# Performance work log

Measured on AMD Instinct MI355X. Metric: run time of the kernel, lower is better.

The kernel has to match this reference:

```python
import jax, jax.numpy as jnp
import numpy as np

N, E = 50000, 800000
IN_DIM, OUT_DIM, REL_DIM = 128, 64, 32
NEG_SLOPE = 0.01  # torch F.leaky_relu default


def setup_inputs() -> dict:
    key = jax.random.key(0)
    ks = jax.random.split(key, 12)
    return {
        "h": jax.random.normal(ks[0], (N, IN_DIM), jnp.float32),
        "relation": jax.random.normal(ks[1], (E, REL_DIM), jnp.float32),
        "score": jax.random.normal(ks[2], (E, 1), jnp.float32),
        "timestamp": jax.random.normal(ks[3], (E, 1), jnp.float32),
        "src": jax.random.randint(ks[4], (E,), 0, N, jnp.int32),
        "dst": jax.random.randint(ks[5], (E,), 0, N, jnp.int32),
        "W_n": jax.random.normal(ks[6], (IN_DIM, OUT_DIM), jnp.float32) / np.sqrt(IN_DIM),
        "W_r": jax.random.normal(ks[7], (REL_DIM, OUT_DIM), jnp.float32) / np.sqrt(REL_DIM),
        "W_s": jax.random.normal(ks[8], (1, OUT_DIM), jnp.float32),
        "W_t": jax.random.normal(ks[9], (1, OUT_DIM), jnp.float32),
        "a": jax.random.normal(ks[10], (5 * OUT_DIM,), jnp.float32) / np.sqrt(5 * OUT_DIM),
    }


def reference(h, relation, score, timestamp, src, dst, W_n, W_r, W_s, W_t, a):
    D = W_n.shape[1]
    z = h @ W_n                     # (N, D)
    er = relation @ W_r             # (E, D)
    es = score @ W_s                # (E, D)
    et = timestamp @ W_t            # (E, D)
    z_src = z[src]                  # (E, D) gather
    z_dst = z[dst]                  # (E, D) gather
    # attn_fc on concat([z_src, z_dst, er, es, et]) == sum of slice dot-products
    a1, a2, a3, a4, a5 = (a[0:D], a[D:2*D], a[2*D:3*D], a[3*D:4*D], a[4*D:5*D])
    logit = z_src @ a1 + z_dst @ a2 + er @ a3 + es @ a4 + et @ a5  # (E,)
    logit = jnp.where(logit >= 0, logit, NEG_SLOPE * logit)        # leaky_relu
    # segment softmax over edges grouped by dst node
    n = z.shape[0]
    seg_max = jax.ops.segment_max(logit, dst, num_segments=n)     # (N,)
    ex = jnp.exp(logit - seg_max[dst])                             # (E,)
    seg_sum = jax.ops.segment_sum(ex, dst, num_segments=n)        # (N,)
    alpha = ex / seg_sum[dst]                                      # (E,)
    # weighted scatter-sum of source features to dst nodes
    h_out = jax.ops.segment_sum(alpha[:, None] * z_src, dst, num_segments=n)  # (N, D)
    return h_out
```

## Files before the change

### kernel.cpp

```cpp
#include <hip/hip_runtime.h>

#define IN_DIM 128
#define OUT_DIM 64
#define REL_DIM 32
#define NEG_SLOPE 0.01f
#define CAP 64
#define FB_EDGES 2048
#define BCAP 1536
#define MAXB 1024

__global__ __launch_bounds__(256) void k_node(const float* __restrict__ h,
                                              const float* __restrict__ W_n,
                                              const float* __restrict__ a,
                                              float* __restrict__ z,
                                              float* __restrict__ s1,
                                              float* __restrict__ s2,
                                              int* __restrict__ bcnt, int n) {
    __shared__ float hs[IN_DIM * 65];
    __shared__ float s1p[4][64], s2p[4][64];
    int base = blockIdx.x * 64;

    if (blockIdx.x == 0)
        for (int i = threadIdx.x; i < MAXB; i += 256) bcnt[i] = 0;

    for (int i = threadIdx.x; i < 64 * 32; i += 256) {
        int r = i >> 5;
        int c4 = i & 31;
        float4 v = make_float4(0.f, 0.f, 0.f, 0.f);
        if (base + r < n) v = ((const float4*)(h + (size_t)(base + r) * IN_DIM))[c4];
        int k0 = c4 * 4;
        hs[(k0 + 0) * 65 + r] = v.x;
        hs[(k0 + 1) * 65 + r] = v.y;
        hs[(k0 + 2) * 65 + r] = v.z;
        hs[(k0 + 3) * 65 + r] = v.w;
    }
    __syncthreads();

    int lane = threadIdx.x & 63;
    int w = __builtin_amdgcn_readfirstlane(threadIdx.x >> 6);
    int c0 = w * 16;
    int row = base + lane;

    float acc[16];
    #pragma unroll
    for (int j = 0; j < 16; ++j) acc[j] = 0.f;

    const float* __restrict__ Wslice = W_n + c0;
    #pragma unroll 4
    for (int k = 0; k < IN_DIM; ++k) {
        float hv = hs[k * 65 + lane];
        const float* __restrict__ Wr = Wslice + k * OUT_DIM;
        #pragma unroll
        for (int j = 0; j < 16; ++j) acc[j] = fmaf(hv, Wr[j], acc[j]);
    }

    float p1 = 0.f, p2 = 0.f;
    #pragma unroll
    for (int j = 0; j < 16; ++j) {
        p1 = fmaf(acc[j], a[c0 + j], p1);
        p2 = fmaf(acc[j], a[OUT_DIM + c0 + j], p2);
    }
    s1p[w][lane] = p1;
    s2p[w][lane] = p2;

    if (row < n) {
        float4* zp = (float4*)(z + (size_t)row * OUT_DIM + c0);
        zp[0] = make_float4(acc[0], acc[1], acc[2], acc[3]);
        zp[1] = make_float4(acc[4], acc[5], acc[6], acc[7]);
        zp[2] = make_float4(acc[8], acc[9], acc[10], acc[11]);
        zp[3] = make_float4(acc[12], acc[13], acc[14], acc[15]);
    }
    __syncthreads();
    if (threadIdx.x < 64 && base + (int)threadIdx.x < n) {
        int l = threadIdx.x;
        s1[base + l] = s1p[0][l] + s1p[1][l] + s1p[2][l] + s1p[3][l];
        s2[base + l] = s2p[0][l] + s2p[1][l] + s2p[2][l] + s2p[3][l];
    }
}

__global__ __launch_bounds__(512) void k_fillP(const float* __restrict__ rel,
                                               const float* __restrict__ score,
                                               const float* __restrict__ ts,
                                               const int* __restrict__ src,
                                               const int* __restrict__ dst,
                                               const float* __restrict__ s1,
                                               const float* __restrict__ s2,
                                               const float* __restrict__ W_r,
                                               const float* __restrict__ W_s,
                                               const float* __restrict__ W_t,
                                               const float* __restrict__ a,
                                               int* __restrict__ bcnt,
                                               int2* __restrict__ rec2,
                                               int E, int nbkt) {
    __shared__ float cw[REL_DIM + 2];
    __shared__ int2  stage[FB_EDGES];
    __shared__ int   sinfo[FB_EDGES];
    __shared__ int   lhist[MAXB];
    __shared__ int   lbase[MAXB];
    int tid = threadIdx.x;

    if (tid < REL_DIM) {
        const float* a3 = a + 2 * OUT_DIM;
        float acc = 0.f;
        #pragma unroll
        for (int d2 = 0; d2 < OUT_DIM; ++d2)
            acc = fmaf(W_r[tid * OUT_DIM + d2], a3[d2], acc);
        cw[tid] = acc;
    } else if (tid == 32) {
        float acc = 0.f;
        for (int d2 = 0; d2 < OUT_DIM; ++d2) acc = fmaf(W_s[d2], a[3 * OUT_DIM + d2], acc);
        cw[32] = acc;
    } else if (tid == 33) {
        float acc = 0.f;
        for (int d2 = 0; d2 < OUT_DIM; ++d2) acc = fmaf(W_t[d2], a[4 * OUT_DIM + d2], acc);
        cw[33] = acc;
    }
    for (int i = tid; i < nbkt; i += 512) lhist[i] = 0;
    __syncthreads();

    int e0 = blockIdx.x * FB_EDGES;
    int g = tid >> 3;
    int sub = tid & 7;

    #pragma unroll 1
    for (int it = 0; it < FB_EDGES / 64; ++it) {
        int le = it * 64 + g;
        int e = e0 + le;
        if (e < E) {
            float4 w4 = ((const float4*)cw)[sub];
            float4 v = ((const float4*)rel)[(size_t)e * 8 + sub];
            float dot = v.x * w4.x + v.y * w4.y + v.z * w4.z + v.w * w4.w;
            dot += __shfl_xor(dot, 1, 8);
            dot += __shfl_xor(dot, 2, 8);
            dot += __shfl_xor(dot, 4, 8);
            if (sub == 0) {
                int s = src[e], d = dst[e];
                float lg = dot + s1[s] + s2[d] + score[e] * cw[32] + ts[e] * cw[33];
                lg = (lg >= 0.f) ? lg : NEG_SLOPE * lg;
                int b = d >> 6;
                int lr = atomicAdd(&lhist[b], 1);
                stage[le] = make_int2((int)(((unsigned)d << 16) | (unsigned)s),
                                      __float_as_int(lg));
                sinfo[le] = (lr << 12) | b;
            }
        }
    }
    __syncthreads();

    for (int b = tid; b < nbkt; b += 512) {
        int c = lhist[b];
        if (c > 0) lbase[b] = atomicAdd(bcnt + b, c);
    }
    __syncthreads();

    for (int le = tid; le < FB_EDGES; le += 512) {
        int e = e0 + le;
        if (e < E) {
            int info = sinfo[le];
            int b = info & 0xFFF;
            int lr = info >> 12;
            int pos = lbase[b] + lr;
            if (pos < BCAP) rec2[(size_t)b * BCAP + pos] = stage[le];
        }
    }
}

__global__ __launch_bounds__(256) void k_out2(const int* __restrict__ bcnt,
                                              const int2* __restrict__ rec2,
                                              const float* __restrict__ z,
                                              float* __restrict__ out, int n) {
    __shared__ int2 seg[64][CAP];
    __shared__ int scnt[64];
    int b = blockIdx.x;
    int tid = threadIdx.x;
    if (tid < 64) scnt[tid] = 0;
    __syncthreads();

    int cnt = bcnt[b];
    if (cnt > BCAP) cnt = BCAP;
    const int2* rb = rec2 + (size_t)b * BCAP;
    for (int i = tid; i < cnt; i += 256) {
        int2 r = rb[i];
        int dl = (int)((((unsigned)r.x) >> 16) & 63u);
        int rk = atomicAdd(&scnt[dl], 1);
        if (rk < CAP) seg[dl][rk] = make_int2(r.x & 0xffff, r.y);
    }
    __syncthreads();

    int lane = tid & 63;
    int w = tid >> 6;
    int eg = lane >> 4;
    int dl4 = lane & 15;
    for (int k = 0; k < 16; ++k) {
        int dl = w * 16 + k;
        int node = b * 64 + dl;
        if (node >= n) break;
        int deg = min(scnt[dl], CAP);
        float4 acc = make_float4(0.f, 0.f, 0.f, 0.f);
        if (deg > 0) {
            int2 pe = make_int2(0, (int)0xff800000u);
            if (lane < deg) pe = seg[dl][lane];
            float v = __int_as_float(pe.y);
            float m = v;
            #pragma unroll
            for (int o = 32; o > 0; o >>= 1) m = fmaxf(m, __shfl_xor(m, o, 64));
            float ex = __expf(v - m);
            float ssum = ex;
            #pragma unroll
            for (int o = 32; o > 0; o >>= 1) ssum += __shfl_xor(ssum, o, 64);
            float alpha = ex * (1.0f / ssum);
            for (int j0 = 0; j0 < deg; j0 += 4) {
                int j = j0 + eg;
                int jc = (j < 64) ? j : 63;
                float wj = __shfl(alpha, jc, 64);
                int sj = __shfl(pe.x, jc, 64);
                if (j < deg) {
                    float4 zv = ((const float4*)(z + (size_t)sj * OUT_DIM))[dl4];
                    acc.x = fmaf(wj, zv.x, acc.x);
                    acc.y = fmaf(wj, zv.y, acc.y);
                    acc.z = fmaf(wj, zv.z, acc.z);
                    acc.w = fmaf(wj, zv.w, acc.w);
                }
            }
        }
        #pragma unroll
        for (int o = 16; o <= 32; o <<= 1) {
            acc.x += __shfl_xor(acc.x, o, 64);
            acc.y += __shfl_xor(acc.y, o, 64);
            acc.z += __shfl_xor(acc.z, o, 64);
            acc.w += __shfl_xor(acc.w, o, 64);
        }
        if (eg == 0) ((float4*)(out + (size_t)node * OUT_DIM))[dl4] = acc;
    }
}

extern "C" void kernel_launch(void* const* d_in, const int* in_sizes, int n_in,
                              void* d_out, int out_size, void* d_ws, size_t ws_size,
                              hipStream_t stream) {
    const float* h         = (const float*)d_in[0];
    const float* relation  = (const float*)d_in[1];
    const float* score     = (const float*)d_in[2];
    const float* timestamp = (const float*)d_in[3];
    const int*   src       = (const int*)d_in[4];
    const int*   dst       = (const int*)d_in[5];
    const float* W_n       = (const float*)d_in[6];
    const float* W_r       = (const float*)d_in[7];
    const float* W_s       = (const float*)d_in[8];
    const float* W_t       = (const float*)d_in[9];
    const float* a         = (const float*)d_in[10];

    int n = in_sizes[0] / IN_DIM;
    int E = in_sizes[4];
    int nbkt = (n + 63) >> 6;

    float* ws   = (float*)d_ws;
    float* z    = ws;
    float* s1   = z + (size_t)n * OUT_DIM;
    float* s2   = s1 + n;
    int*   bcnt = (int*)(s2 + n);
    int2*  rec2 = (int2*)(bcnt + MAXB);

    float* out = (float*)d_out;

    k_node<<<(n + 63) / 64, 256, 0, stream>>>(h, W_n, a, z, s1, s2, bcnt, n);

    int nfb = (E + FB_EDGES - 1) / FB_EDGES;
    k_fillP<<<nfb, 512, 0, stream>>>(relation, score, timestamp, src, dst,
                                     s1, s2, W_r, W_s, W_t, a, bcnt, rec2, E, nbkt);

    k_out2<<<nbkt, 256, 0, stream>>>(bcnt, rec2, z, out, n);
}
```

Baseline: 297.8 us.

## Replace atomic bucket fill with histogram, scan and deterministic scatter passes

Edge bucketing by destination block now runs in three stages: a per-block histogram kernel, a per-bucket exclusive scan across edge blocks, and a scatter kernel that writes records straight to their precomputed offsets. This removes the global atomics on bucket counters and the second shared-memory staging pass. The scatter kernel also preloads src, dst, score and timestamp into shared memory. The output kernel moves to 512 threads with 8 nodes per wave. The cost is two extra launches and a scan kernel that does 1024-thread block syncs for each of about 782 buckets. The fixed HSTRIDE of 800 caps the node count.

```diff
diff --git a/kernel.cpp b/kernel.cpp
--- a/kernel.cpp
+++ b/kernel.cpp
@@ -5,23 +5,19 @@
 #define REL_DIM 32
 #define NEG_SLOPE 0.01f
 #define CAP 64
-#define FB_EDGES 2048
+#define EPB 1024
 #define BCAP 1536
-#define MAXB 1024
+#define HSTRIDE 800
 
 __global__ __launch_bounds__(256) void k_node(const float* __restrict__ h,
                                               const float* __restrict__ W_n,
                                               const float* __restrict__ a,
                                               float* __restrict__ z,
                                               float* __restrict__ s1,
-                                              float* __restrict__ s2,
-                                              int* __restrict__ bcnt, int n) {
+                                              float* __restrict__ s2, int n) {
     __shared__ float hs[IN_DIM * 65];
     __shared__ float s1p[4][64], s2p[4][64];
     int base = blockIdx.x * 64;
-
-    if (blockIdx.x == 0)
-        for (int i = threadIdx.x; i < MAXB; i += 256) bcnt[i] = 0;
 
     for (int i = threadIdx.x; i < 64 * 32; i += 256) {
         int r = i >> 5;
@@ -78,53 +74,101 @@
     }
 }
 
-__global__ __launch_bounds__(512) void k_fillP(const float* __restrict__ rel,
-                                               const float* __restrict__ score,
-                                               const float* __restrict__ ts,
-                                               const int* __restrict__ src,
-                                               const int* __restrict__ dst,
-                                               const float* __restrict__ s1,
-                                               const float* __restrict__ s2,
-                                               const float* __restrict__ W_r,
-                                               const float* __restrict__ W_s,
-                                               const float* __restrict__ W_t,
-                                               const float* __restrict__ a,
-                                               int* __restrict__ bcnt,
-                                               int2* __restrict__ rec2,
-                                               int E, int nbkt) {
-    __shared__ float cw[REL_DIM + 2];
-    __shared__ int2  stage[FB_EDGES];
-    __shared__ int   sinfo[FB_EDGES];
-    __shared__ int   lhist[MAXB];
-    __shared__ int   lbase[MAXB];
-    int tid = threadIdx.x;
-
-    if (tid < REL_DIM) {
+__global__ __launch_bounds__(256) void k_hist(const int* __restrict__ dst,
+                                              int* __restrict__ hist, int E, int nbkt) {
+    __shared__ int lh[HSTRIDE];
+    int t = threadIdx.x;
+    for (int i = t; i < nbkt; i += 256) lh[i] = 0;
+    __syncthreads();
+    int e0 = blockIdx.x * EPB;
+    #pragma unroll
+    for (int i = 0; i < EPB / 256; ++i) {
+        int e = e0 + i * 256 + t;
+        if (e < E) atomicAdd(&lh[dst[e] >> 6], 1);
+    }
+    __syncthreads();
+    for (int b = t; b < nbkt; b += 256)
+        hist[(size_t)blockIdx.x * HSTRIDE + b] = lh[b];
+}
+
+__global__ __launch_bounds__(1024) void k_scan(int* __restrict__ hist,
+                                               int* __restrict__ bcnt, int nblk) {
+    __shared__ int tmp[1024];
+    int b = blockIdx.x;
+    int t = threadIdx.x;
+    int v = (t < nblk) ? hist[(size_t)t * HSTRIDE + b] : 0;
+    tmp[t] = v;
+    __syncthreads();
+    #pragma unroll
+    for (int o = 1; o < 1024; o <<= 1) {
+        int x = (t >= o) ? tmp[t - o] : 0;
+        __syncthreads();
+        tmp[t] += x;
+        __syncthreads();
+    }
+    if (t < nblk) hist[(size_t)t * HSTRIDE + b] = tmp[t] - v;
+    if (t == 0) bcnt[b] = tmp[1023];
+}
+
+__global__ __launch_bounds__(256) void k_scatter(const float* __restrict__ rel,
+                                                 const float* __restrict__ score,
+                                                 const float* __restrict__ ts,
+                                                 const int* __restrict__ src,
+                                                 const int* __restrict__ dst,
+                                                 const float* __restrict__ s1,
+                                                 const float* __restrict__ s2,
+                                                 const float* __restrict__ W_r,
+                                                 const float* __restrict__ W_s,
+                                                 const float* __restrict__ W_t,
+                                                 const float* __restrict__ a,
+                                                 const int* __restrict__ hist,
+                                                 int2* __restrict__ rec2,
+                                                 int E, int nbkt) {
+    __shared__ __align__(16) float cw[36];
+    __shared__ int   lsrc[EPB], ldst[EPB];
+    __shared__ float lsc[EPB],  lts[EPB];
+    __shared__ int   lrank[HSTRIDE], lbase[HSTRIDE];
+    int t = threadIdx.x;
+    int e0 = blockIdx.x * EPB;
+
+    if (t < REL_DIM) {
         const float* a3 = a + 2 * OUT_DIM;
         float acc = 0.f;
         #pragma unroll
         for (int d2 = 0; d2 < OUT_DIM; ++d2)
-            acc = fmaf(W_r[tid * OUT_DIM + d2], a3[d2], acc);
-        cw[tid] = acc;
-    } else if (tid == 32) {
+            acc = fmaf(W_r[t * OUT_DIM + d2], a3[d2], acc);
+        cw[t] = acc;
+    } else if (t == 32) {
         float acc = 0.f;
         for (int d2 = 0; d2 < OUT_DIM; ++d2) acc = fmaf(W_s[d2], a[3 * OUT_DIM + d2], acc);
         cw[32] = acc;
-    } else if (tid == 33) {
+    } else if (t == 33) {
         float acc = 0.f;
         for (int d2 = 0; d2 < OUT_DIM; ++d2) acc = fmaf(W_t[d2], a[4 * OUT_DIM + d2], acc);
         cw[33] = acc;
     }
-    for (int i = tid; i < nbkt; i += 512) lhist[i] = 0;
-    __syncthreads();
-
-    int e0 = blockIdx.x * FB_EDGES;
-    int g = tid >> 3;
-    int sub = tid & 7;
-
+    for (int i = t; i < nbkt; i += 256) {
+        lrank[i] = 0;
+        lbase[i] = hist[(size_t)blockIdx.x * HSTRIDE + i];
+    }
+    #pragma unroll
+    for (int i = 0; i < EPB / 256; ++i) {
+        int le = i * 256 + t;
+        int e = e0 + le;
+        if (e < E) {
+            lsrc[le] = src[e];
+            ldst[le] = dst[e];
+            lsc[le]  = score[e];
+            lts[le]  = ts[e];
+        }
+    }
+    __syncthreads();
+
+    int g = t >> 3;
+    int sub = t & 7;
     #pragma unroll 1
-    for (int it = 0; it < FB_EDGES / 64; ++it) {
-        int le = it * 64 + g;
+    for (int it = 0; it < EPB / 32; ++it) {
+        int le = it * 32 + g;
         int e = e0 + le;
         if (e < E) {
             float4 w4 = ((const float4*)cw)[sub];
@@ -134,38 +178,22 @@
             dot += __shfl_xor(dot, 2, 8);
             dot += __shfl_xor(dot, 4, 8);
             if (sub == 0) {
-                int s = src[e], d = dst[e];
-                float lg = dot + s1[s] + s2[d] + score[e] * cw[32] + ts[e] * cw[33];
+                int s = lsrc[le], d = ldst[le];
+                float lg = dot + s1[s] + s2[d] + lsc[le] * cw[32] + lts[le] * cw[33];
                 lg = (lg >= 0.f) ? lg : NEG_SLOPE * lg;
                 int b = d >> 6;
-                int lr = atomicAdd(&lhist[b], 1);
-                stage[le] = make_int2((int)(((unsigned)d << 16) | (unsigned)s),
-                                      __float_as_int(lg));
-                sinfo[le] = (lr << 12) | b;
+                int lr = atomicAdd(&lrank[b], 1);
+                int pos = lbase[b] + lr;
+                if (pos < BCAP)
+                    rec2[(size_t)b * BCAP + pos] =
+                        make_int2((int)(((unsigned)d << 16) | (unsigned)s),
+                                  __float_as_int(lg));
             }
         }
     }
-    __syncthreads();
-
-    for (int b = tid; b < nbkt; b += 512) {
-        int c = lhist[b];
-        if (c > 0) lbase[b] = atomicAdd(bcnt + b, c);
-    }
-    __syncthreads();
-
-    for (int le = tid; le < FB_EDGES; le += 512) {
-        int e = e0 + le;
-        if (e < E) {
-            int info = sinfo[le];
-            int b = info & 0xFFF;
-            int lr = info >> 12;
-            int pos = lbase[b] + lr;
-            if (pos < BCAP) rec2[(size_t)b * BCAP + pos] = stage[le];
-        }
-    }
-}
-
-__global__ __launch_bounds__(256) void k_out2(const int* __restrict__ bcnt,
+}
+
+__global__ __launch_bounds__(512) void k_out2(const int* __restrict__ bcnt,
                                               const int2* __restrict__ rec2,
                                               const float* __restrict__ z,
                                               float* __restrict__ out, int n) {
@@ -179,7 +207,7 @@
     int cnt = bcnt[b];
     if (cnt > BCAP) cnt = BCAP;
     const int2* rb = rec2 + (size_t)b * BCAP;
-    for (int i = tid; i < cnt; i += 256) {
+    for (int i = tid; i < cnt; i += 512) {
         int2 r = rb[i];
         int dl = (int)((((unsigned)r.x) >> 16) & 63u);
         int rk = atomicAdd(&scnt[dl], 1);
@@ -191,8 +219,8 @@
     int w = tid >> 6;
     int eg = lane >> 4;
     int dl4 = lane & 15;
-    for (int k = 0; k < 16; ++k) {
-        int dl = w * 16 + k;
+    for (int k = 0; k < 8; ++k) {
+        int dl = w * 8 + k;
         int node = b * 64 + dl;
         if (node >= n) break;
         int deg = min(scnt[dl], CAP);
@@ -252,21 +280,22 @@
     int n = in_sizes[0] / IN_DIM;
     int E = in_sizes[4];
     int nbkt = (n + 63) >> 6;
+    int nblk = (E + EPB - 1) / EPB;
 
     float* ws   = (float*)d_ws;
     float* z    = ws;
     float* s1   = z + (size_t)n * OUT_DIM;
     float* s2   = s1 + n;
     int*   bcnt = (int*)(s2 + n);
-    int2*  rec2 = (int2*)(bcnt + MAXB);
+    int*   hist = bcnt + HSTRIDE;
+    int2*  rec2 = (int2*)(hist + (size_t)nblk * HSTRIDE);
 
     float* out = (float*)d_out;
 
-    k_node<<<(n + 63) / 64, 256, 0, stream>>>(h, W_n, a, z, s1, s2, bcnt, n);
-
-    int nfb = (E + FB_EDGES - 1) / FB_EDGES;
-    k_fillP<<<nfb, 512, 0, stream>>>(relation, score, timestamp, src, dst,
-                                     s1, s2, W_r, W_s, W_t, a, bcnt, rec2, E, nbkt);
-
-    k_out2<<<nbkt, 256, 0, stream>>>(bcnt, rec2, z, out, n);
-}
+    k_node<<<(n + 63) / 64, 256, 0, stream>>>(h, W_n, a, z, s1, s2, n);
+    k_hist<<<nblk, 256, 0, stream>>>(dst, hist, E, nbkt);
+    k_scan<<<nbkt, 1024, 0, stream>>>(hist, bcnt, nblk);
+    k_scatter<<<nblk, 256, 0, stream>>>(relation, score, timestamp, src, dst,
+                                        s1, s2, W_r, W_s, W_t, a, hist, rec2, E, nbkt);
+    k_out2<<<nbkt, 512, 0, stream>>>(bcnt, rec2, z, out, n);
+}
```

Result: no change. 295.8 us (-0.7%).
